# Optimization experiments

Hardware: AMD Instinct MI355X
Metric: run time of the kernel (lower is better)

## Reference

```python
import jax, jax.numpy as jnp
import numpy as np

NUM_REGIONS = 29
OUT = 7          # RoIAlign output size
SR = 2           # sampling_ratio
IMG = 1024.0     # input image H = W
LN_EPS = 1e-5


def _layernorm(x, g, b):
    mu = jnp.mean(x, axis=-1, keepdims=True)
    var = jnp.mean(jnp.square(x - mu), axis=-1, keepdims=True)
    return (x - mu) * jax.lax.rsqrt(var + LN_EPS) * g + b


def _roi_align(fm, rois):
    """torchvision roi_align (aligned=False), spatial_scale=1.0, sampling_ratio=SR.
    fm: [B,C,H,W], rois: [B,R,4] (x1,y1,x2,y2 in feature coords). -> [B,R,C,OUT,OUT]"""
    B, C, H, W = fm.shape
    x1, y1, x2, y2 = jnp.moveaxis(rois, -1, 0)            # each [B,R]
    roi_w = jnp.maximum(x2 - x1, 1.0)
    roi_h = jnp.maximum(y2 - y1, 1.0)
    bw = roi_w / OUT
    bh = roi_h / OUT
    # sub-bin offsets: (bin + (s+0.5)/SR) for bin in [0,OUT), s in [0,SR)
    off = jnp.arange(OUT, dtype=jnp.float32)[:, None] + (jnp.arange(SR, dtype=jnp.float32)[None, :] + 0.5) / SR  # [OUT,SR]
    py = y1[..., None, None] + off * bh[..., None, None]  # [B,R,OUT,SR]
    px = x1[..., None, None] + off * bw[..., None, None]  # [B,R,OUT,SR]
    y = py[:, :, :, :, None, None]                        # [B,R,OUT,SR,1,1]
    x = px[:, :, None, None, :, :]                        # [B,R,1,1,OUT,SR]
    valid = (y >= -1.0) & (y <= H) & (x >= -1.0) & (x <= W)
    yc = jnp.clip(y, 0.0, H - 1.0)
    xc = jnp.clip(x, 0.0, W - 1.0)
    y0 = jnp.floor(yc).astype(jnp.int32)
    x0 = jnp.floor(xc).astype(jnp.int32)
    y1i = jnp.minimum(y0 + 1, H - 1)
    x1i = jnp.minimum(x0 + 1, W - 1)
    ly = yc - y0
    lx = xc - x0
    hy = 1.0 - ly
    hx = 1.0 - lx
    gather = jax.vmap(lambda f, yy, xx: f[:, yy, xx])     # per image: [C,H,W] -> [C,...]
    v00 = gather(fm, y0, x0)                              # [B,C,R,OUT,SR,OUT,SR]
    v01 = gather(fm, y0, x1i)
    v10 = gather(fm, y1i, x0)
    v11 = gather(fm, y1i, x1i)
    w00 = (hy * hx)[:, None]
    w01 = (hy * lx)[:, None]
    w10 = (ly * hx)[:, None]
    w11 = (ly * lx)[:, None]
    val = w00 * v00 + w01 * v01 + w10 * v10 + w11 * v11
    val = jnp.where(valid[:, None], val, 0.0)
    pooled = val.mean(axis=(4, 6))                        # average over SRxSR samples -> [B,C,R,OUT,OUT]
    return jnp.transpose(pooled, (0, 2, 1, 3, 4))         # [B,R,C,OUT,OUT]


def setup_inputs() -> dict:
    key = jax.random.key(0)
    ks = jax.random.split(key, 8)
    B, N, C, Hf, Wf, FD = 32, 40, 256, 64, 64, 768
    D = C * OUT * OUT
    feature_maps = jax.random.normal(ks[0], (B, C, Hf, Wf), jnp.float32)
    xy = jax.random.uniform(ks[1], (B, N, 2), jnp.float32) * 900.0
    wh = jax.random.uniform(ks[2], (B, N, 2), jnp.float32) * 100.0 + 16.0
    boxes = jnp.concatenate([xy, xy + wh], axis=-1)       # valid x1,y1,x2,y2 in image coords
    scores = jax.random.uniform(ks[3], (B, N), jnp.float32)
    labels = jax.random.randint(ks[4], (B, N), 0, NUM_REGIONS + 1)
    return {
        'feature_maps': feature_maps,
        'boxes': boxes,
        'scores': scores,
        'labels': labels,
        'w1': jax.random.normal(ks[5], (D, 2048), jnp.float32) * 0.02,
        'b1': jnp.zeros((2048,), jnp.float32),
        'g1': jnp.ones((2048,), jnp.float32),
        'be1': jnp.zeros((2048,), jnp.float32),
        'w2': jax.random.normal(ks[6], (2048, FD), jnp.float32) * 0.02,
        'b2': jnp.zeros((FD,), jnp.float32),
        'g2': jnp.ones((FD,), jnp.float32),
        'be2': jnp.zeros((FD,), jnp.float32),
        'missing_token': jax.random.normal(ks[7], (FD,), jnp.float32),
    }


def reference(feature_maps, boxes, scores, labels, w1, b1, g1, be1, w2, b2, g2, be2, missing_token):
    B, C, Hf, Wf = feature_maps.shape
    R = NUM_REGIONS
    scale = jnp.minimum(Hf / IMG, Wf / IMG)               # scale_factors (same for all images)
    # segmented argmax: best-scoring box per (image, region)
    region_idx = jnp.clip(labels, 1, R) - 1               # [B,N]
    onehot = region_idx[..., None] == jnp.arange(R)       # [B,N,R]
    masked = jnp.where(onehot, scores[..., None], -1.0)   # init best score = -1.0
    detected = jnp.any(onehot, axis=1)                    # [B,R]
    best = jnp.argmax(masked, axis=1)                     # [B,R] first max, matches strict-> loop
    sel = jnp.take_along_axis(boxes, jnp.broadcast_to(best[:, :, None], (B, R, 4)), axis=1)
    rois = sel * scale                                    # [B,R,4] in feature-map coords
    roi_feats = _roi_align(feature_maps, rois)            # [B,R,C,7,7]
    flat = roi_feats.reshape(B * R, C * OUT * OUT)
    h = _layernorm(flat @ w1 + b1, g1, be1)
    h = jax.nn.relu(h)
    h = _layernorm(h @ w2 + b2, g2, be2)                  # [B*R, feature_dim]
    feats = h.reshape(B, R, -1)
    region_features = jnp.where(detected[..., None], feats, missing_token)
    return region_features, detected
```

## Files before the change

### kernel.cpp

```cpp
#include <hip/hip_runtime.h>

typedef __bf16 bf16x8 __attribute__((ext_vector_type(8)));
typedef float f32x4 __attribute__((ext_vector_type(4)));
typedef unsigned short ushort8v __attribute__((ext_vector_type(8)));
typedef unsigned short ushort4v __attribute__((ext_vector_type(4)));

#define BATCH 32
#define NBOX 40
#define CCH 256
#define HF 64
#define WF 64
#define RREG 29
#define OUTP 7
#define MROWS 928
#define DDIM 12544
#define N1DIM 2048
#define FDIM 768
#define PDIM 4096
#define S1 8
#define S2 8

static constexpr size_t OFF_ROIS = 0;
static constexpr size_t OFF_DET  = 16384;
static constexpr size_t OFF_A    = 32768;
static constexpr size_t OFF_W1T  = OFF_A   + (size_t)MROWS * DDIM * 2;
static constexpr size_t OFF_FMT  = OFF_W1T;
static constexpr size_t OFF_W2T  = OFF_W1T + (size_t)DDIM * N1DIM * 2;
static constexpr size_t OFF_GP   = OFF_W2T + (size_t)N1DIM * FDIM * 2;
static constexpr size_t OFF_H    = OFF_W1T;

static __device__ __forceinline__ unsigned short f2bf(float f) {
  __bf16 h = (__bf16)f;
  return __builtin_bit_cast(unsigned short, h);
}
static __device__ __forceinline__ float bf2f(unsigned short u) {
  unsigned int x = ((unsigned int)u) << 16;
  return __builtin_bit_cast(float, x);
}
static __device__ __forceinline__ void gload_lds16(const void* g, void* l) {
  __builtin_amdgcn_global_load_lds((const __attribute__((address_space(1))) void*)g,
                                   (__attribute__((address_space(3))) void*)l, 16, 0, 0);
}

__global__ __launch_bounds__(256) void selfmt_kernel(const float* __restrict__ in,
                                                     unsigned short* __restrict__ out,
                                                     const float* __restrict__ boxes,
                                                     const float* __restrict__ scores,
                                                     const int* __restrict__ labels,
                                                     float* __restrict__ rois,
                                                     int* __restrict__ det,
                                                     float* __restrict__ out_det) {
  __shared__ float tile[64][65];
  int bid = blockIdx.x;
  int t = threadIdx.x;
  if (bid >= PDIM / 64 * (CCH / 64) * BATCH) {
    int tid = (bid - PDIM / 64 * (CCH / 64) * BATCH) * 256 + t;
    if (tid >= MROWS) return;
    int b = tid / RREG, r = tid % RREG;
    float bestS = -1.0f;
    int bestN = 0;
    int found = 0;
    for (int n = 0; n < NBOX; ++n) {
      int lab = labels[b * NBOX + n];
      int ri = min(max(lab, 1), RREG) - 1;
      if (ri == r) {
        found = 1;
        float s = scores[b * NBOX + n];
        if (s > bestS) { bestS = s; bestN = n; }
      }
    }
    const float scale = 0.0625f;
    float4 bx = *(const float4*)&boxes[(b * NBOX + bestN) * 4];
    rois[tid * 4 + 0] = bx.x * scale;
    rois[tid * 4 + 1] = bx.y * scale;
    rois[tid * 4 + 2] = bx.z * scale;
    rois[tid * 4 + 3] = bx.w * scale;
    det[tid] = found;
    out_det[tid] = found ? 1.0f : 0.0f;
    return;
  }
  int p0 = (bid & 63) * 64, c0 = ((bid >> 6) & 3) * 64, b = bid >> 8;
  int tx = t & 15, ty = t >> 4;
#pragma unroll
  for (int q = 0; q < 4; ++q) {
    int r = ty + q * 16;
    float4 v = *(const float4*)&in[((long)b * CCH + c0 + r) * PDIM + p0 + tx * 4];
    tile[r][tx * 4 + 0] = v.x;
    tile[r][tx * 4 + 1] = v.y;
    tile[r][tx * 4 + 2] = v.z;
    tile[r][tx * 4 + 3] = v.w;
  }
  __syncthreads();
#pragma unroll
  for (int q = 0; q < 4; ++q) {
    int r = ty + q * 16;
    ushort4v o;
    o[0] = f2bf(tile[tx * 4 + 0][r]);
    o[1] = f2bf(tile[tx * 4 + 1][r]);
    o[2] = f2bf(tile[tx * 4 + 2][r]);
    o[3] = f2bf(tile[tx * 4 + 3][r]);
    *(ushort4v*)&out[((long)b * PDIM + p0 + r) * CCH + c0 + tx * 4] = o;
  }
}

__global__ __launch_bounds__(256) void roi_kernel(const unsigned short* __restrict__ fmT,
                                                  const float* __restrict__ rois,
                                                  unsigned short* __restrict__ A) {
  __shared__ int sidx[196][4];
  __shared__ float swt[196][4];
  __shared__ unsigned short Arow[DDIM];
  int roi = blockIdx.x;
  int t = threadIdx.x;
  float rx1 = rois[roi * 4 + 0], ry1 = rois[roi * 4 + 1];
  float rx2 = rois[roi * 4 + 2], ry2 = rois[roi * 4 + 3];
  float roiw = fmaxf(rx2 - rx1, 1.f), roih = fmaxf(ry2 - ry1, 1.f);
  float bw = roiw * (1.f / OUTP), bh = roih * (1.f / OUTP);
  if (t < 196) {
    int oy = t / 28, rem = t % 28, ox = rem / 4, s = rem % 4, sy = s >> 1, sx = s & 1;
    float y = ry1 + ((float)oy + ((float)sy + 0.5f) * 0.5f) * bh;
    float x = rx1 + ((float)ox + ((float)sx + 0.5f) * 0.5f) * bw;
    bool valid = (y >= -1.f) && (y <= 64.f) && (x >= -1.f) && (x <= 64.f);
    float yc = fminf(fmaxf(y, 0.f), 63.f);
    float xc = fminf(fmaxf(x, 0.f), 63.f);
    int y0 = (int)floorf(yc), x0 = (int)floorf(xc);
    int y1i = min(y0 + 1, 63), x1i = min(x0 + 1, 63);
    float ly = yc - (float)y0, lx = xc - (float)x0;
    float hy = 1.f - ly, hx = 1.f - lx;
    float m = valid ? 1.f : 0.f;
    swt[t][0] = hy * hx * m;
    swt[t][1] = hy * lx * m;
    swt[t][2] = ly * hx * m;
    swt[t][3] = ly * lx * m;
    sidx[t][0] = (y0 * 64 + x0) * CCH;
    sidx[t][1] = (y0 * 64 + x1i) * CCH;
    sidx[t][2] = (y1i * 64 + x0) * CCH;
    sidx[t][3] = (y1i * 64 + x1i) * CCH;
  }
  __syncthreads();
  int b = roi / RREG;
  int cg = t & 63;
  int sub = t >> 6;
  int start = sub * 12 + min(sub, 1);
  int cnt = sub == 0 ? 13 : 12;
  const unsigned short* base = fmT + (long)b * PDIM * CCH + cg * 4;
  for (int bi = 0; bi < cnt; ++bi) {
    int bin = start + bi;
    float a0 = 0.f, a1 = 0.f, a2 = 0.f, a3 = 0.f;
#pragma unroll
    for (int s = 0; s < 4; ++s) {
      int sid = bin * 4 + s;
#pragma unroll
      for (int tp = 0; tp < 4; ++tp) {
        float w = swt[sid][tp];
        ushort4v v = *(const ushort4v*)(base + sidx[sid][tp]);
        a0 += w * bf2f(v[0]);
        a1 += w * bf2f(v[1]);
        a2 += w * bf2f(v[2]);
        a3 += w * bf2f(v[3]);
      }
    }
    Arow[(cg * 4 + 0) * 49 + bin] = f2bf(a0 * 0.25f);
    Arow[(cg * 4 + 1) * 49 + bin] = f2bf(a1 * 0.25f);
    Arow[(cg * 4 + 2) * 49 + bin] = f2bf(a2 * 0.25f);
    Arow[(cg * 4 + 3) * 49 + bin] = f2bf(a3 * 0.25f);
  }
  __syncthreads();
  const ushort8v* src = (const ushort8v*)Arow;
  ushort8v* dst = (ushort8v*)(A + (long)roi * DDIM);
  for (int i = t; i < DDIM / 8; i += 256) dst[i] = src[i];
}

__global__ __launch_bounds__(256) void wT_kernel(const float* __restrict__ w1,
                                                 unsigned short* __restrict__ w1t,
                                                 const float* __restrict__ w2,
                                                 unsigned short* __restrict__ w2t) {
  __shared__ float tile[64][65];
  int bid = blockIdx.x;
  const float* in;
  unsigned short* out;
  int K, N, k0, n0;
  if (bid < (DDIM / 64) * (N1DIM / 64)) {
    in = w1; out = w1t; K = DDIM; N = N1DIM;
    k0 = (bid % (DDIM / 64)) * 64;
    n0 = (bid / (DDIM / 64)) * 64;
  } else {
    int r = bid - (DDIM / 64) * (N1DIM / 64);
    in = w2; out = w2t; K = N1DIM; N = FDIM;
    k0 = (r % (N1DIM / 64)) * 64;
    n0 = (r / (N1DIM / 64)) * 64;
  }
  int t = threadIdx.x, tx = t & 15, ty = t >> 4;
#pragma unroll
  for (int p = 0; p < 4; ++p) {
    int r = ty + p * 16;
    float4 v = *(const float4*)&in[(long)(k0 + r) * N + n0 + tx * 4];
    tile[r][tx * 4 + 0] = v.x;
    tile[r][tx * 4 + 1] = v.y;
    tile[r][tx * 4 + 2] = v.z;
    tile[r][tx * 4 + 3] = v.w;
  }
  __syncthreads();
#pragma unroll
  for (int p = 0; p < 4; ++p) {
    int r = ty + p * 16;
    ushort4v o;
    o[0] = f2bf(tile[tx * 4 + 0][r]);
    o[1] = f2bf(tile[tx * 4 + 1][r]);
    o[2] = f2bf(tile[tx * 4 + 2][r]);
    o[3] = f2bf(tile[tx * 4 + 3][r]);
    *(ushort4v*)&out[(long)(n0 + r) * K + k0 + tx * 4] = o;
  }
}

__global__ __launch_bounds__(256, 2) void gemm_sk_kernel(const unsigned short* __restrict__ A,
                                                         const unsigned short* __restrict__ Bt,
                                                         float* __restrict__ Cp,
                                                         int M, int N, int K, int kchunk,
                                                         int gy, int q) {
  __shared__ unsigned short As[2 * 128 * 64];
  __shared__ unsigned short Bs[2 * 128 * 64];
  int bid = blockIdx.x;
  int tile = (bid & 7) * q + (bid >> 3);
  int bm = tile & 7;
  int rest = tile >> 3;
  int bn = rest % gy;
  int s = rest / gy;

  int t = threadIdx.x;
  int lane = t & 63, wv = t >> 6;
  int wr = wv >> 1, wc = wv & 1;
  int fr = lane & 15, fq = lane >> 4;

  f32x4 acc[4][4];
#pragma unroll
  for (int m = 0; m < 4; ++m)
#pragma unroll
    for (int n = 0; n < 4; ++n) acc[m][n] = (f32x4){0.f, 0.f, 0.f, 0.f};

  int srow = t >> 3;
  int scol = t & 7;
  int k_begin = s * kchunk;
  int k_end = min(k_begin + kchunk, K);
  int nkt = (k_end - k_begin) >> 6;

  int garow[4], gbrow[4], schunk[4];
#pragma unroll
  for (int i = 0; i < 4; ++i) {
    int row = srow + i * 32;
    schunk[i] = (scol ^ (row & 7)) * 8;
    garow[i] = min(bm * 128 + row, M - 1);
    gbrow[i] = bn * 128 + row;
  }

#define GSTAGE(buf, kt_) do {                                                  \
    int k0_ = k_begin + (kt_) * 64;                                            \
    _Pragma("unroll")                                                          \
    for (int i = 0; i < 4; ++i)                                                \
      gload_lds16(A + (long)garow[i] * K + k0_ + schunk[i],                    \
                  (char*)As + (buf) * 16384 + t * 16 + i * 4096);              \
    _Pragma("unroll")                                                          \
    for (int i = 0; i < 4; ++i)                                                \
      gload_lds16(Bt + (long)gbrow[i] * K + k0_ + schunk[i],                   \
                  (char*)Bs + (buf) * 16384 + t * 16 + i * 4096);              \
  } while (0)

  GSTAGE(0, 0);
  GSTAGE(1, min(1, nkt - 1));

  for (int kt = 0; kt < nkt; ++kt) {
    int cur = kt & 1;
    asm volatile("s_waitcnt vmcnt(8)" ::: "memory");
    __builtin_amdgcn_sched_barrier(0);
    __builtin_amdgcn_s_barrier();
    __builtin_amdgcn_sched_barrier(0);

    const char* Ab = (const char*)As + cur * 16384;
    const char* Bb = (const char*)Bs + cur * 16384;
#pragma unroll
    for (int ks = 0; ks < 2; ++ks) {
      bf16x8 af[4], bfv[4];
#pragma unroll
      for (int m = 0; m < 4; ++m) {
        int row = wr * 64 + m * 16 + fr;
        int bc = (ks * 64 + fq * 16) ^ ((row & 7) << 4);
        af[m] = *(const bf16x8*)(Ab + row * 128 + bc);
      }
#pragma unroll
      for (int n = 0; n < 4; ++n) {
        int row = wc * 64 + n * 16 + fr;
        int bc = (ks * 64 + fq * 16) ^ ((row & 7) << 4);
        bfv[n] = *(const bf16x8*)(Bb + row * 128 + bc);
      }
#pragma unroll
      for (int m = 0; m < 4; ++m)
#pragma unroll
        for (int n = 0; n < 4; ++n)
          acc[m][n] = __builtin_amdgcn_mfma_f32_16x16x32_bf16(af[m], bfv[n], acc[m][n], 0, 0, 0);
    }

    __builtin_amdgcn_sched_barrier(0);
    __builtin_amdgcn_s_barrier();
    __builtin_amdgcn_sched_barrier(0);
    GSTAGE(cur, min(kt + 2, nkt - 1));
  }
#undef GSTAGE

  float* Cb = Cp + (long)s * M * N;
#pragma unroll
  for (int m = 0; m < 4; ++m)
#pragma unroll
    for (int n = 0; n < 4; ++n) {
      int col = bn * 128 + wc * 64 + n * 16 + fr;
#pragma unroll
      for (int j = 0; j < 4; ++j) {
        int row = bm * 128 + wr * 64 + m * 16 + fq * 4 + j;
        if (row < M) Cb[(long)row * N + col] = acc[m][n][j];
      }
    }
}

static __device__ __forceinline__ void block_reduce2(float& a, float& b, float* sm) {
#pragma unroll
  for (int off = 32; off > 0; off >>= 1) {
    a += __shfl_down(a, off);
    b += __shfl_down(b, off);
  }
  int lane = threadIdx.x & 63, wv = threadIdx.x >> 6;
  if (lane == 0) { sm[wv] = a; sm[wv + 4] = b; }
  __syncthreads();
  a = sm[0] + sm[1] + sm[2] + sm[3];
  b = sm[4] + sm[5] + sm[6] + sm[7];
}

__global__ __launch_bounds__(256) void ln1_kernel(const float* __restrict__ X,
                                                  const float* __restrict__ b1,
                                                  const float* __restrict__ g1,
                                                  const float* __restrict__ be1,
                                                  unsigned short* __restrict__ H) {
  __shared__ float sm[8];
  int row = blockIdx.x, t = threadIdx.x;
  float x[8];
  float sum = 0.f, sq = 0.f;
#pragma unroll
  for (int i = 0; i < 8; ++i) {
    int j = t + i * 256;
    float v = b1[j];
#pragma unroll
    for (int s = 0; s < S1; ++s) v += X[((long)s * MROWS + row) * N1DIM + j];
    x[i] = v;
    sum += v;
    sq += v * v;
  }
  block_reduce2(sum, sq, sm);
  float mu = sum * (1.f / N1DIM);
  float inv = rsqrtf(sq * (1.f / N1DIM) - mu * mu + 1e-5f);
#pragma unroll
  for (int i = 0; i < 8; ++i) {
    int j = t + i * 256;
    float y = fmaxf((x[i] - mu) * inv * g1[j] + be1[j], 0.f);
    H[(long)row * N1DIM + j] = f2bf(y);
  }
}

__global__ __launch_bounds__(256) void ln2_kernel(const float* __restrict__ X,
                                                  const float* __restrict__ b2,
                                                  const float* __restrict__ g2,
                                                  const float* __restrict__ be2,
                                                  const float* __restrict__ miss,
                                                  const int* __restrict__ det,
                                                  float* __restrict__ out) {
  __shared__ float sm[8];
  int row = blockIdx.x, t = threadIdx.x;
  float x[3];
  float sum = 0.f, sq = 0.f;
#pragma unroll
  for (int i = 0; i < 3; ++i) {
    int j = t + i * 256;
    float v = b2[j];
#pragma unroll
    for (int s = 0; s < S2; ++s) v += X[((long)s * MROWS + row) * FDIM + j];
    x[i] = v;
    sum += v;
    sq += v * v;
  }
  block_reduce2(sum, sq, sm);
  float mu = sum * (1.f / FDIM);
  float inv = rsqrtf(sq * (1.f / FDIM) - mu * mu + 1e-5f);
  int dv = det[row];
#pragma unroll
  for (int i = 0; i < 3; ++i) {
    int j = t + i * 256;
    float y = (x[i] - mu) * inv * g2[j] + be2[j];
    out[(long)row * FDIM + j] = dv ? y : miss[j];
  }
}

extern "C" void kernel_launch(void* const* d_in, const int* in_sizes, int n_in,
                              void* d_out, int out_size, void* d_ws, size_t ws_size,
                              hipStream_t stream) {
  const float* fm     = (const float*)d_in[0];
  const float* boxes  = (const float*)d_in[1];
  const float* scores = (const float*)d_in[2];
  const int*   labels = (const int*)d_in[3];
  const float* w1     = (const float*)d_in[4];
  const float* b1     = (const float*)d_in[5];
  const float* g1     = (const float*)d_in[6];
  const float* be1    = (const float*)d_in[7];
  const float* w2     = (const float*)d_in[8];
  const float* b2     = (const float*)d_in[9];
  const float* g2     = (const float*)d_in[10];
  const float* be2    = (const float*)d_in[11];
  const float* miss   = (const float*)d_in[12];
  float* out = (float*)d_out;
  char* ws = (char*)d_ws;

  float* rois = (float*)(ws + OFF_ROIS);
  int* det = (int*)(ws + OFF_DET);
  unsigned short* Abf = (unsigned short*)(ws + OFF_A);
  unsigned short* fmT = (unsigned short*)(ws + OFF_FMT);
  unsigned short* w1t = (unsigned short*)(ws + OFF_W1T);
  unsigned short* w2t = (unsigned short*)(ws + OFF_W2T);
  float* Gp = (float*)(ws + OFF_GP);
  unsigned short* Hbf = (unsigned short*)(ws + OFF_H);

  hipLaunchKernelGGL(selfmt_kernel, dim3(8192 + 4), dim3(256), 0, stream,
                     fm, fmT, boxes, scores, labels, rois, det, out + (long)MROWS * FDIM);
  hipLaunchKernelGGL(roi_kernel, dim3(MROWS), dim3(256), 0, stream, fmT, rois, Abf);
  hipLaunchKernelGGL(wT_kernel, dim3((DDIM / 64) * (N1DIM / 64) + (N1DIM / 64) * (FDIM / 64)),
                     dim3(256), 0, stream, w1, w1t, w2, w2t);
  {
    int nkb = DDIM / 64;
    int kc = ((nkb + S1 - 1) / S1) * 64;
    int gy = N1DIM / 128, nwg = 8 * gy * S1;
    hipLaunchKernelGGL(gemm_sk_kernel, dim3(nwg), dim3(256), 0, stream,
                       Abf, w1t, Gp, MROWS, N1DIM, DDIM, kc, gy, nwg / 8);
  }
  hipLaunchKernelGGL(ln1_kernel, dim3(MROWS), dim3(256), 0, stream, Gp, b1, g1, be1, Hbf);
  {
    int nkb = N1DIM / 64;
    int kc = ((nkb + S2 - 1) / S2) * 64;
    int gy = FDIM / 128, nwg = 8 * gy * S2;
    hipLaunchKernelGGL(gemm_sk_kernel, dim3(nwg), dim3(256), 0, stream,
                       Hbf, w2t, Gp, MROWS, FDIM, N1DIM, kc, gy, nwg / 8);
  }
  hipLaunchKernelGGL(ln2_kernel, dim3(MROWS), dim3(256), 0, stream,
                     Gp, b2, g2, be2, miss, det, out);
}
```

Measured before the change: 190.0 us.

## Fuse feature-map bf16 conversion into RoIAlign with LDS-resident channel planes

Drops the separate transpose/convert pass that wrote a channel-last bf16 copy of the feature map. Each workgroup now loads 8 fp32 channel planes of one image into LDS as bf16 and runs RoIAlign for all 29 regions of that image from shared memory. This removes a full write and re-read of the transposed feature map and the scattered global gathers. In exchange it uses about 64KB of LDS per block, which limits occupancy, adds two barriers per region, and issues narrow 2-byte stores to A.

```diff
diff --git a/kernel.cpp b/kernel.cpp
--- a/kernel.cpp
+++ b/kernel.cpp
@@ -24,7 +24,6 @@
 static constexpr size_t OFF_DET  = 16384;
 static constexpr size_t OFF_A    = 32768;
 static constexpr size_t OFF_W1T  = OFF_A   + (size_t)MROWS * DDIM * 2;
-static constexpr size_t OFF_FMT  = OFF_W1T;
 static constexpr size_t OFF_W2T  = OFF_W1T + (size_t)DDIM * N1DIM * 2;
 static constexpr size_t OFF_GP   = OFF_W2T + (size_t)N1DIM * FDIM * 2;
 static constexpr size_t OFF_H    = OFF_W1T;
@@ -42,132 +41,93 @@
                                    (__attribute__((address_space(3))) void*)l, 16, 0, 0);
 }
 
-__global__ __launch_bounds__(256) void selfmt_kernel(const float* __restrict__ in,
-                                                     unsigned short* __restrict__ out,
-                                                     const float* __restrict__ boxes,
+__global__ __launch_bounds__(256) void select_kernel(const float* __restrict__ boxes,
                                                      const float* __restrict__ scores,
                                                      const int* __restrict__ labels,
                                                      float* __restrict__ rois,
                                                      int* __restrict__ det,
                                                      float* __restrict__ out_det) {
-  __shared__ float tile[64][65];
-  int bid = blockIdx.x;
+  int tid = blockIdx.x * 256 + threadIdx.x;
+  if (tid >= MROWS) return;
+  int b = tid / RREG, r = tid % RREG;
+  float bestS = -1.0f;
+  int bestN = 0;
+  int found = 0;
+  for (int n = 0; n < NBOX; ++n) {
+    int lab = labels[b * NBOX + n];
+    int ri = min(max(lab, 1), RREG) - 1;
+    if (ri == r) {
+      found = 1;
+      float s = scores[b * NBOX + n];
+      if (s > bestS) { bestS = s; bestN = n; }
+    }
+  }
+  const float scale = 0.0625f;
+  float4 bx = *(const float4*)&boxes[(b * NBOX + bestN) * 4];
+  rois[tid * 4 + 0] = bx.x * scale;
+  rois[tid * 4 + 1] = bx.y * scale;
+  rois[tid * 4 + 2] = bx.z * scale;
+  rois[tid * 4 + 3] = bx.w * scale;
+  det[tid] = found;
+  out_det[tid] = found ? 1.0f : 0.0f;
+}
+
+__global__ __launch_bounds__(256) void roialign_kernel(const float* __restrict__ fm,
+                                                       const float* __restrict__ rois,
+                                                       unsigned short* __restrict__ A) {
+  __shared__ unsigned short planes[8][4104];
+  __shared__ int4 sidx[196];
+  __shared__ float4 swt[196];
+  int b = blockIdx.x;
+  int cg = blockIdx.y;
   int t = threadIdx.x;
-  if (bid >= PDIM / 64 * (CCH / 64) * BATCH) {
-    int tid = (bid - PDIM / 64 * (CCH / 64) * BATCH) * 256 + t;
-    if (tid >= MROWS) return;
-    int b = tid / RREG, r = tid % RREG;
-    float bestS = -1.0f;
-    int bestN = 0;
-    int found = 0;
-    for (int n = 0; n < NBOX; ++n) {
-      int lab = labels[b * NBOX + n];
-      int ri = min(max(lab, 1), RREG) - 1;
-      if (ri == r) {
-        found = 1;
-        float s = scores[b * NBOX + n];
-        if (s > bestS) { bestS = s; bestN = n; }
+
+  const float4* src = (const float4*)(fm + ((long)b * CCH + cg * 8) * PDIM);
+  for (int i = t; i < 8192; i += 256) {
+    int pl = i >> 10, off = (i & 1023) * 4;
+    float4 v = src[i];
+    ushort4v o = {f2bf(v.x), f2bf(v.y), f2bf(v.z), f2bf(v.w)};
+    *(ushort4v*)&planes[pl][off] = o;
+  }
+
+  for (int r = 0; r < RREG; ++r) {
+    __syncthreads();
+    int roi = b * RREG + r;
+    if (t < 196) {
+      float rx1 = rois[roi * 4 + 0], ry1 = rois[roi * 4 + 1];
+      float rx2 = rois[roi * 4 + 2], ry2 = rois[roi * 4 + 3];
+      float roiw = fmaxf(rx2 - rx1, 1.f), roih = fmaxf(ry2 - ry1, 1.f);
+      float bw = roiw * (1.f / OUTP), bh = roih * (1.f / OUTP);
+      int oy = t / 28, rem = t % 28, ox = rem / 4, s = rem % 4, sy = s >> 1, sx = s & 1;
+      float y = ry1 + ((float)oy + ((float)sy + 0.5f) * 0.5f) * bh;
+      float x = rx1 + ((float)ox + ((float)sx + 0.5f) * 0.5f) * bw;
+      bool valid = (y >= -1.f) && (y <= 64.f) && (x >= -1.f) && (x <= 64.f);
+      float yc = fminf(fmaxf(y, 0.f), 63.f);
+      float xc = fminf(fmaxf(x, 0.f), 63.f);
+      int y0 = (int)floorf(yc), x0 = (int)floorf(xc);
+      int y1i = min(y0 + 1, 63), x1i = min(x0 + 1, 63);
+      float ly = yc - (float)y0, lx = xc - (float)x0;
+      float hy = 1.f - ly, hx = 1.f - lx;
+      float m = valid ? 1.f : 0.f;
+      swt[t] = make_float4(hy * hx * m, hy * lx * m, ly * hx * m, ly * lx * m);
+      sidx[t] = make_int4(y0 * 64 + x0, y0 * 64 + x1i, y1i * 64 + x0, y1i * 64 + x1i);
+    }
+    __syncthreads();
+    long abase = (long)roi * DDIM + (long)cg * 8 * 49;
+    for (int idx = t; idx < 392; idx += 256) {
+      int cl = idx / 49, bin = idx - cl * 49;
+      float acc = 0.f;
+#pragma unroll
+      for (int s = 0; s < 4; ++s) {
+        int sid = bin * 4 + s;
+        int4 ix = sidx[sid];
+        float4 w = swt[sid];
+        acc += w.x * bf2f(planes[cl][ix.x]) + w.y * bf2f(planes[cl][ix.y])
+             + w.z * bf2f(planes[cl][ix.z]) + w.w * bf2f(planes[cl][ix.w]);
       }
+      A[abase + idx] = f2bf(acc * 0.25f);
     }
-    const float scale = 0.0625f;
-    float4 bx = *(const float4*)&boxes[(b * NBOX + bestN) * 4];
-    rois[tid * 4 + 0] = bx.x * scale;
-    rois[tid * 4 + 1] = bx.y * scale;
-    rois[tid * 4 + 2] = bx.z * scale;
-    rois[tid * 4 + 3] = bx.w * scale;
-    det[tid] = found;
-    out_det[tid] = found ? 1.0f : 0.0f;
-    return;
-  }
-  int p0 = (bid & 63) * 64, c0 = ((bid >> 6) & 3) * 64, b = bid >> 8;
-  int tx = t & 15, ty = t >> 4;
-#pragma unroll
-  for (int q = 0; q < 4; ++q) {
-    int r = ty + q * 16;
-    float4 v = *(const float4*)&in[((long)b * CCH + c0 + r) * PDIM + p0 + tx * 4];
-    tile[r][tx * 4 + 0] = v.x;
-    tile[r][tx * 4 + 1] = v.y;
-    tile[r][tx * 4 + 2] = v.z;
-    tile[r][tx * 4 + 3] = v.w;
-  }
-  __syncthreads();
-#pragma unroll
-  for (int q = 0; q < 4; ++q) {
-    int r = ty + q * 16;
-    ushort4v o;
-    o[0] = f2bf(tile[tx * 4 + 0][r]);
-    o[1] = f2bf(tile[tx * 4 + 1][r]);
-    o[2] = f2bf(tile[tx * 4 + 2][r]);
-    o[3] = f2bf(tile[tx * 4 + 3][r]);
-    *(ushort4v*)&out[((long)b * PDIM + p0 + r) * CCH + c0 + tx * 4] = o;
-  }
-}
-
-__global__ __launch_bounds__(256) void roi_kernel(const unsigned short* __restrict__ fmT,
-                                                  const float* __restrict__ rois,
-                                                  unsigned short* __restrict__ A) {
-  __shared__ int sidx[196][4];
-  __shared__ float swt[196][4];
-  __shared__ unsigned short Arow[DDIM];
-  int roi = blockIdx.x;
-  int t = threadIdx.x;
-  float rx1 = rois[roi * 4 + 0], ry1 = rois[roi * 4 + 1];
-  float rx2 = rois[roi * 4 + 2], ry2 = rois[roi * 4 + 3];
-  float roiw = fmaxf(rx2 - rx1, 1.f), roih = fmaxf(ry2 - ry1, 1.f);
-  float bw = roiw * (1.f / OUTP), bh = roih * (1.f / OUTP);
-  if (t < 196) {
-    int oy = t / 28, rem = t % 28, ox = rem / 4, s = rem % 4, sy = s >> 1, sx = s & 1;
-    float y = ry1 + ((float)oy + ((float)sy + 0.5f) * 0.5f) * bh;
-    float x = rx1 + ((float)ox + ((float)sx + 0.5f) * 0.5f) * bw;
-    bool valid = (y >= -1.f) && (y <= 64.f) && (x >= -1.f) && (x <= 64.f);
-    float yc = fminf(fmaxf(y, 0.f), 63.f);
-    float xc = fminf(fmaxf(x, 0.f), 63.f);
-    int y0 = (int)floorf(yc), x0 = (int)floorf(xc);
-    int y1i = min(y0 + 1, 63), x1i = min(x0 + 1, 63);
-    float ly = yc - (float)y0, lx = xc - (float)x0;
-    float hy = 1.f - ly, hx = 1.f - lx;
-    float m = valid ? 1.f : 0.f;
-    swt[t][0] = hy * hx * m;
-    swt[t][1] = hy * lx * m;
-    swt[t][2] = ly * hx * m;
-    swt[t][3] = ly * lx * m;
-    sidx[t][0] = (y0 * 64 + x0) * CCH;
-    sidx[t][1] = (y0 * 64 + x1i) * CCH;
-    sidx[t][2] = (y1i * 64 + x0) * CCH;
-    sidx[t][3] = (y1i * 64 + x1i) * CCH;
-  }
-  __syncthreads();
-  int b = roi / RREG;
-  int cg = t & 63;
-  int sub = t >> 6;
-  int start = sub * 12 + min(sub, 1);
-  int cnt = sub == 0 ? 13 : 12;
-  const unsigned short* base = fmT + (long)b * PDIM * CCH + cg * 4;
-  for (int bi = 0; bi < cnt; ++bi) {
-    int bin = start + bi;
-    float a0 = 0.f, a1 = 0.f, a2 = 0.f, a3 = 0.f;
-#pragma unroll
-    for (int s = 0; s < 4; ++s) {
-      int sid = bin * 4 + s;
-#pragma unroll
-      for (int tp = 0; tp < 4; ++tp) {
-        float w = swt[sid][tp];
-        ushort4v v = *(const ushort4v*)(base + sidx[sid][tp]);
-        a0 += w * bf2f(v[0]);
-        a1 += w * bf2f(v[1]);
-        a2 += w * bf2f(v[2]);
-        a3 += w * bf2f(v[3]);
-      }
-    }
-    Arow[(cg * 4 + 0) * 49 + bin] = f2bf(a0 * 0.25f);
-    Arow[(cg * 4 + 1) * 49 + bin] = f2bf(a1 * 0.25f);
-    Arow[(cg * 4 + 2) * 49 + bin] = f2bf(a2 * 0.25f);
-    Arow[(cg * 4 + 3) * 49 + bin] = f2bf(a3 * 0.25f);
-  }
-  __syncthreads();
-  const ushort8v* src = (const ushort8v*)Arow;
-  ushort8v* dst = (ushort8v*)(A + (long)roi * DDIM);
-  for (int i = t; i < DDIM / 8; i += 256) dst[i] = src[i];
+  }
 }
 
 __global__ __launch_bounds__(256) void wT_kernel(const float* __restrict__ w1,
@@ -417,15 +377,15 @@
   float* rois = (float*)(ws + OFF_ROIS);
   int* det = (int*)(ws + OFF_DET);
   unsigned short* Abf = (unsigned short*)(ws + OFF_A);
-  unsigned short* fmT = (unsigned short*)(ws + OFF_FMT);
   unsigned short* w1t = (unsigned short*)(ws + OFF_W1T);
   unsigned short* w2t = (unsigned short*)(ws + OFF_W2T);
   float* Gp = (float*)(ws + OFF_GP);
   unsigned short* Hbf = (unsigned short*)(ws + OFF_H);
 
-  hipLaunchKernelGGL(selfmt_kernel, dim3(8192 + 4), dim3(256), 0, stream,
-                     fm, fmT, boxes, scores, labels, rois, det, out + (long)MROWS * FDIM);
-  hipLaunchKernelGGL(roi_kernel, dim3(MROWS), dim3(256), 0, stream, fmT, rois, Abf);
+  hipLaunchKernelGGL(select_kernel, dim3(4), dim3(256), 0, stream,
+                     boxes, scores, labels, rois, det, out + (long)MROWS * FDIM);
+  hipLaunchKernelGGL(roialign_kernel, dim3(BATCH, CCH / 8), dim3(256), 0, stream,
+                     fm, rois, Abf);
   hipLaunchKernelGGL(wT_kernel, dim3((DDIM / 64) * (N1DIM / 64) + (N1DIM / 64) * (FDIM / 64)),
                      dim3(256), 0, stream, w1, w1t, w2, w2t);
   {
```

Result: slower. 273.6 us (+44.0%).
